# Optimization experiments

Hardware: AMD Instinct MI355X
Metric: run time of the kernel (lower is better)

Reference implementation:

```python
import jax, jax.numpy as jnp
import numpy as np
from functools import partial

# ---- constants from params ----
NODES = 64          # cfg_s[0]: nodes per graph
HEADS, BASES = 8, 4 # EGConv num_heads / num_bases (aggregators = ['symnorm'], A=1)
THRESH, LENS = 0.5, 0.5
ENC_THRESH, ENC_LENS = 0.5, 0.5
DECAY = 0.2
LSTM_ALPHA = 2.0

# ---- surrogate spike functions ----
@partial(jax.custom_vjp, nondiff_argnums=(1, 2))
def atan_spike(x, thresh, alpha):
    return (x > thresh).astype(x.dtype)

def _atan_fwd(x, thresh, alpha):
    return atan_spike(x, thresh, alpha), x

def _atan_bwd(thresh, alpha, x, g):
    grad = (alpha / 2.0) / (1.0 + (jnp.pi / 2.0 * alpha * (x - thresh)) ** 2)
    return (g * grad,)

atan_spike.defvjp(_atan_fwd, _atan_bwd)

@partial(jax.custom_vjp, nondiff_argnums=(1,))
def erf_spike(x, alpha):
    return (x > 0).astype(x.dtype)

def _erf_fwd(x, alpha):
    return erf_spike(x, alpha), x

def _erf_bwd(alpha, x, g):
    grad = alpha / (2.0 * jnp.sqrt(jnp.pi)) * jnp.exp(-(alpha * x / 2.0) ** 2)
    return (g * grad,)

erf_spike.defvjp(_erf_fwd, _erf_bwd)


def setup_inputs() -> dict:
    key = jax.random.key(0)
    N, Cin, T = 16384, 8, 32
    Cenc, Cgnn = 128, 128
    Fh = Cgnn // HEADS
    HID, FC1, NC = 512, 256, 4
    E = 262144
    ks = jax.random.split(key, 12)

    def w(k, shape, fan_in):
        return jax.random.normal(k, shape, jnp.float32) / np.float32(np.sqrt(fan_in))

    return {
        "x": jax.random.normal(ks[0], (N, Cin, T), jnp.float32),
        "edge_index": jax.random.randint(ks[1], (2, E), 0, N, dtype=jnp.int32),
        "enc_W": w(ks[2], (Cin, Cenc), Cin),
        "enc_b": jnp.zeros((Cenc,), jnp.float32),
        "bases_W": w(ks[3], (Cenc, BASES * Fh), Cenc),
        "bases_b": jnp.zeros((BASES * Fh,), jnp.float32),
        "comb_W": w(ks[4], (Cenc, HEADS * BASES), Cenc),
        "comb_b": jnp.zeros((HEADS * BASES,), jnp.float32),
        "conv_bias": jnp.zeros((Cgnn,), jnp.float32),
        "W_ih": w(ks[5], (NODES * Cgnn, 4 * HID), NODES * Cgnn),
        "W_hh": w(ks[6], (HID, 4 * HID), HID),
        "b_ih": jnp.zeros((4 * HID,), jnp.float32),
        "b_hh": jnp.zeros((4 * HID,), jnp.float32),
        "fc1_W": w(ks[7], (HID, FC1), HID),
        "fc1_b": jnp.zeros((FC1,), jnp.float32),
        "fc2_W": w(ks[8], (FC1, NC), FC1),
        "fc2_b": jnp.zeros((NC,), jnp.float32),
    }


def reference(x, edge_index, enc_W, enc_b, bases_W, bases_b, comb_W, comb_b,
              conv_bias, W_ih, W_hh, b_ih, b_hh, fc1_W, fc1_b, fc2_W, fc2_b):
    N, Cin, T = x.shape
    S = N // NODES
    Cgnn = conv_bias.shape[0]
    Fh = Cgnn // HEADS
    HID = W_hh.shape[0]
    FC1 = fc1_b.shape[0]
    NC = fc2_b.shape[0]

    # EGConv symnorm graph structure with self-loops (fixed across time)
    loop = jnp.arange(N, dtype=edge_index.dtype)
    s_all = jnp.concatenate([edge_index[0], loop])
    d_all = jnp.concatenate([edge_index[1], loop])
    deg = jax.ops.segment_sum(jnp.ones(s_all.shape[0], x.dtype), d_all, num_segments=N)
    dinv = jnp.where(deg > 0, jax.lax.rsqrt(jnp.maximum(deg, 1e-12)), 0.0)
    ew = dinv[s_all] * dinv[d_all]  # [E+N]

    xs = jnp.moveaxis(x, -1, 0)  # [T, N, Cin]

    def step(carry, xt):
        (enc_mem, enc_spike, c1_mem, c1_spike, lh, lc,
         h1_mem, h1_spike, h2_mem, h2_spike, h2_sum) = carry
        # encoding LIF
        enc_mem = enc_mem * DECAY * (1.0 - enc_spike) + xt @ enc_W + enc_b
        enc_spike = atan_spike(enc_mem, ENC_THRESH, ENC_LENS)
        # EGConv (symnorm aggregator, A=1)
        bases = enc_spike @ bases_W + bases_b                       # [N, B*Fh]
        agg = jax.ops.segment_sum(ew[:, None] * bases[s_all], d_all, num_segments=N)
        comb = (enc_spike @ comb_W + comb_b).reshape(N, HEADS, BASES)
        conv = jnp.einsum('nhb,nbf->nhf', comb, agg.reshape(N, BASES, Fh))
        conv = conv.reshape(S, NODES, Cgnn) + conv_bias
        # conv LIF
        c1_mem = c1_mem * DECAY * (1.0 - c1_spike) + conv
        c1_spike = atan_spike(c1_mem, THRESH, LENS)
        # spiking LSTM cell (erf surrogates on all gates)
        xl = c1_spike.reshape(S, NODES * Cgnn)
        gates = xl @ W_ih + b_ih + lh @ W_hh + b_hh
        i, f, g, o = jnp.split(gates, 4, axis=-1)
        i = erf_spike(i, LSTM_ALPHA)
        f = erf_spike(f, LSTM_ALPHA)
        g = erf_spike(g, LSTM_ALPHA)
        o = erf_spike(o, LSTM_ALPHA)
        lc = f * lc + i * g
        lh = lc * o
        # fc1 LIF
        h1_mem = h1_mem * DECAY * (1.0 - h1_spike) + lh @ fc1_W + fc1_b
        h1_spike = atan_spike(h1_mem, THRESH, LENS)
        # fc2 LIF
        h2_mem = h2_mem * DECAY * (1.0 - h2_spike) + h1_spike @ fc2_W + fc2_b
        h2_spike = atan_spike(h2_mem, THRESH, LENS)
        return (enc_mem, enc_spike, c1_mem, c1_spike, lh, lc,
                h1_mem, h1_spike, h2_mem, h2_spike, h2_sum + h2_spike), None

    Cenc = enc_b.shape[0]
    z = lambda shape: jnp.zeros(shape, x.dtype)
    carry0 = (z((N, Cenc)), z((N, Cenc)), z((S, NODES, Cgnn)), z((S, NODES, Cgnn)),
              z((S, HID)), z((S, HID)), z((S, FC1)), z((S, FC1)),
              z((S, NC)), z((S, NC)), z((S, NC)))
    carry, _ = jax.lax.scan(step, carry0, xs)
    h2_sum = carry[-1]
    return h2_sum / jnp.asarray(T, x.dtype)
```

## Files before the change

### kernel.cpp

```cpp
#include <hip/hip_runtime.h>

#define NN      16384
#define TSTEPS  32
#define SG      256
#define NE      262144
#define NPANEL  24
#define GSTRIDE 524288u

#define OFF_ENC_MEM   0u
#define OFF_ENC_SPK   2097152u
#define OFF_C1_MEM    4194304u
#define OFF_C1_SPK    6291456u
#define OFF_LH        8388608u
#define OFF_LC        8519680u
#define OFF_H1_MEM    8650752u
#define OFF_H1_SPK    8716288u
#define OFF_H2_MEM    8781824u
#define OFF_H2_SPK    8782848u
#define OFF_H2_SUM    8783872u
#define ZERO_FLOATS   8784896u
#define OFF_BASES     8784896u
#define OFF_COMB      9833472u
#define OFF_GATES     10357760u
#define OFF_PART      10882048u
#define OFF_DINV      23464960u
#define OFF_COLW      23481344u
#define FLOAT_END     23743488u
#define IOFF_DEG      0
#define IOFF_FILL     16384
#define IOFF_ROWPTR   32768
#define IOFF_EID      49153
#define IOFF_COL      311297
#define INT_COUNT     573441

__global__ void k_deg(const int* __restrict__ ei, int* __restrict__ deg) {
  int e = blockIdx.x * 256 + threadIdx.x;
  if (e < NE) atomicAdd(&deg[ei[NE + e]], 1);
}

__global__ void k_dinv(const int* __restrict__ deg, float* __restrict__ dinv) {
  int n = blockIdx.x * 256 + threadIdx.x;
  if (n < NN) dinv[n] = __fdiv_rn(1.0f, __fsqrt_rn((float)(deg[n] + 1)));
}

__global__ void k_scan(const int* __restrict__ deg, int* __restrict__ rowp) {
  __shared__ int sdata[1024];
  int tid = threadIdx.x;
  int base = tid * 16;
  int loc[16];
  int sum = 0;
  #pragma unroll
  for (int i = 0; i < 16; ++i) { loc[i] = sum; sum += deg[base + i]; }
  sdata[tid] = sum;
  __syncthreads();
  for (int off = 1; off < 1024; off <<= 1) {
    int v = 0;
    if (tid >= off) v = sdata[tid - off];
    __syncthreads();
    sdata[tid] += v;
    __syncthreads();
  }
  int excl = (tid == 0) ? 0 : sdata[tid - 1];
  #pragma unroll
  for (int i = 0; i < 16; ++i) rowp[base + i] = excl + loc[i];
  if (tid == 1023) rowp[NN] = sdata[1023];
}

__global__ void k_scatter(const int* __restrict__ ei, const int* __restrict__ rowp,
                          int* __restrict__ fill, int* __restrict__ eid) {
  int e = blockIdx.x * 256 + threadIdx.x;
  if (e >= NE) return;
  int d = ei[NE + e];
  int pos = rowp[d] + atomicAdd(&fill[d], 1);
  eid[pos] = e;
}

__global__ void k_sortadj(const int* __restrict__ rowp, int* __restrict__ eid,
                          const int* __restrict__ ei, const float* __restrict__ dinv,
                          int* __restrict__ col, float* __restrict__ colw) {
  int d = blockIdx.x * 256 + threadIdx.x;
  if (d >= NN) return;
  int r0 = rowp[d], r1 = rowp[d + 1];
  for (int i = r0 + 1; i < r1; ++i) {
    int key = eid[i];
    int j = i - 1;
    while (j >= r0 && eid[j] > key) { eid[j + 1] = eid[j]; --j; }
    eid[j + 1] = key;
  }
  for (int i = r0; i < r1; ++i) {
    int s = ei[eid[i]];
    col[i] = s;
    colw[i] = dinv[s];
  }
}

__global__ __launch_bounds__(512) void k_bases_comb(
    const float* __restrict__ x, const float* __restrict__ encW, const float* __restrict__ encB,
    float* __restrict__ enc_mem, float* __restrict__ enc_spk,
    const float* __restrict__ basesW, const float* __restrict__ basesB,
    const float* __restrict__ combW, const float* __restrict__ combB,
    float* __restrict__ bases, float* __restrict__ comb, int t) {
  __shared__ float xs[64][8];
  __shared__ float sp[64 * 129];
  __shared__ float ob[64 * 65];
  __shared__ float oc[64 * 33];
  const int tid = threadIdx.x;
  const int nb = blockIdx.x * 64;
  {
    int n = tid >> 3, c = tid & 7;
    xs[n][c] = x[(size_t)(nb + n) * 256 + (size_t)c * 32 + t];
  }
  __syncthreads();
  #pragma unroll 4
  for (int k = 0; k < 16; ++k) {
    int idx = k * 512 + tid;
    int n = idx >> 7, j = idx & 127;
    int gidx = nb * 128 + idx;
    float dot = 0.f;
    #pragma unroll
    for (int c = 0; c < 8; ++c) dot = __fmaf_rn(xs[n][c], encW[c * 128 + j], dot);
    float m = enc_mem[gidx], s = enc_spk[gidx];
    float nm = __fadd_rn(__fadd_rn(__fmul_rn(__fmul_rn(m, 0.2f), __fsub_rn(1.f, s)), dot), encB[j]);
    enc_mem[gidx] = nm;
    float spk = nm > 0.5f ? 1.f : 0.f;
    enc_spk[gidx] = spk;
    sp[n * 129 + j] = spk;
  }
  __syncthreads();
  const int lane = tid & 63;
  const int w = tid >> 6;
  const float* spn = sp + lane * 129;
  if (w < 4) {
    const int ch0 = w * 16;
    const float* Wp = basesW + ch0;
    float acc[16];
    #pragma unroll
    for (int c = 0; c < 16; ++c) acc[c] = 0.f;
    for (int j = 0; j < 128; ++j) {
      const float s = spn[j];
      const float* wr = Wp + j * 64;
      #pragma unroll
      for (int c = 0; c < 16; ++c) acc[c] = __fmaf_rn(s, wr[c], acc[c]);
    }
    #pragma unroll
    for (int c = 0; c < 16; ++c) ob[lane * 65 + ch0 + c] = acc[c];
  } else {
    const int ch0 = (w - 4) * 8;
    const float* Wp = combW + ch0;
    float acc[8];
    #pragma unroll
    for (int c = 0; c < 8; ++c) acc[c] = 0.f;
    for (int j = 0; j < 128; ++j) {
      const float s = spn[j];
      const float* wr = Wp + j * 32;
      #pragma unroll
      for (int c = 0; c < 8; ++c) acc[c] = __fmaf_rn(s, wr[c], acc[c]);
    }
    #pragma unroll
    for (int c = 0; c < 8; ++c) oc[lane * 33 + ch0 + c] = acc[c];
  }
  __syncthreads();
  #pragma unroll
  for (int r = 0; r < 8; ++r) {
    int idx = r * 512 + tid;
    int n = idx >> 6, ch = idx & 63;
    bases[(size_t)(nb + n) * 64 + ch] = __fadd_rn(ob[n * 65 + ch], basesB[ch]);
  }
  #pragma unroll
  for (int r = 0; r < 4; ++r) {
    int idx = r * 512 + tid;
    int n = idx >> 5, ch = idx & 31;
    comb[(size_t)(nb + n) * 32 + ch] = __fadd_rn(oc[n * 33 + ch], combB[ch]);
  }
}

__global__ __launch_bounds__(256) void k_aggconv(
    const float* __restrict__ bases, const float* __restrict__ comb,
    const float* __restrict__ dinv, const int* __restrict__ rowp,
    const int* __restrict__ col, const float* __restrict__ colw,
    const float* __restrict__ convB,
    float* __restrict__ c1_mem, float* __restrict__ c1_spk) {
  __shared__ float aggl[4][64];
  __shared__ float combl[4][32];
  int w = threadIdx.x >> 6;
  int m = threadIdx.x & 63;
  int d = blockIdx.x * 4 + w;
  float dd = dinv[d];
  int r0 = rowp[d], r1 = rowp[d + 1];
  float acc = 0.f;
  int r = r0;
  for (; r + 4 <= r1; r += 4) {
    const int s0 = col[r], s1 = col[r + 1], s2 = col[r + 2], s3 = col[r + 3];
    const float w0 = colw[r], w1 = colw[r + 1], w2 = colw[r + 2], w3 = colw[r + 3];
    const float b0 = bases[(size_t)s0 * 64 + m];
    const float b1 = bases[(size_t)s1 * 64 + m];
    const float b2 = bases[(size_t)s2 * 64 + m];
    const float b3 = bases[(size_t)s3 * 64 + m];
    acc = __fadd_rn(acc, __fmul_rn(__fmul_rn(w0, dd), b0));
    acc = __fadd_rn(acc, __fmul_rn(__fmul_rn(w1, dd), b1));
    acc = __fadd_rn(acc, __fmul_rn(__fmul_rn(w2, dd), b2));
    acc = __fadd_rn(acc, __fmul_rn(__fmul_rn(w3, dd), b3));
  }
  for (; r < r1; ++r) {
    int s = col[r];
    float ew  = __fmul_rn(colw[r], dd);
    float upd = __fmul_rn(ew, bases[(size_t)s * 64 + m]);
    acc = __fadd_rn(acc, upd);
  }
  {
    float ew  = __fmul_rn(dd, dd);
    float upd = __fmul_rn(ew, bases[(size_t)d * 64 + m]);
    acc = __fadd_rn(acc, upd);
  }
  aggl[w][m] = acc;
  if (m < 32) combl[w][m] = comb[(size_t)d * 32 + m];
  __syncthreads();
  #pragma unroll
  for (int half = 0; half < 2; ++half) {
    int j = m + half * 64;
    int h = j >> 4, f = j & 15;
    float cv = 0.f;
    #pragma unroll
    for (int b = 0; b < 4; ++b)
      cv = __fadd_rn(cv, __fmul_rn(combl[w][h * 4 + b], aggl[w][b * 16 + f]));
    cv = __fadd_rn(cv, convB[j]);
    int idx = d * 128 + j;
    float cm = c1_mem[idx], cs = c1_spk[idx];
    float nm = __fadd_rn(__fmul_rn(__fmul_rn(cm, 0.2f), __fsub_rn(1.f, cs)), cv);
    c1_mem[idx] = nm;
    c1_spk[idx] = nm > 0.5f ? 1.f : 0.f;
  }
}

__global__ __launch_bounds__(512) void k_gpanel(
    const float* __restrict__ xl, const float* __restrict__ lh,
    const float* __restrict__ Wih, const float* __restrict__ Whh,
    float* __restrict__ part) {
  __shared__ __align__(16) float Ast[2][16][132];
  __shared__ __align__(16) float Bs[2][16][132];
  const int tid = threadIdx.x;
  const int tx = tid & 31;
  const int ty = tid >> 5;
  const int n0 = blockIdx.x * 128;
  const int m0 = blockIdx.y * 128;
  const int z  = blockIdx.z;

  const float* Asrc; const float* Bsrc; int lda, k0, klen;
  if (z < 22) { Asrc = xl; Bsrc = Wih; lda = 8192; k0 = z * 384; klen = (z == 21) ? 128 : 384; }
  else        { Asrc = lh; Bsrc = Whh; lda = 512;  k0 = (z == 22) ? 0 : 384; klen = (z == 22) ? 384 : 128; }

  float acc[8][4];
  #pragma unroll
  for (int i = 0; i < 8; ++i)
    #pragma unroll
    for (int j = 0; j < 4; ++j) acc[i][j] = 0.f;

  const int arow = tid >> 2;
  const int acol = (tid & 3) * 4;
  const int brow = tid >> 5;
  const int bcol = (tid & 31) * 4;

  const int nkt = klen >> 4;

  float4 va, vb;

  va = *(const float4*)(Asrc + (size_t)(m0 + arow) * lda + k0 + acol);
  vb = *(const float4*)(Bsrc + (size_t)(k0 + brow) * 2048 + n0 + bcol);
  Ast[0][acol + 0][arow] = va.x; Ast[0][acol + 1][arow] = va.y;
  Ast[0][acol + 2][arow] = va.z; Ast[0][acol + 3][arow] = va.w;
  *(float4*)&Bs[0][brow][bcol] = vb;
  __syncthreads();

  for (int kt = 0; kt < nkt; ++kt) {
    const int cur = kt & 1;
    const bool more = (kt + 1 < nkt);
    if (more) {
      const int kb = k0 + ((kt + 1) << 4);
      va = *(const float4*)(Asrc + (size_t)(m0 + arow) * lda + kb + acol);
      vb = *(const float4*)(Bsrc + (size_t)(kb + brow) * 2048 + n0 + bcol);
    }
    #pragma unroll
    for (int kk = 0; kk < 16; ++kk) {
      const float4 a0 = *(const float4*)&Ast[cur][kk][ty * 8];
      const float4 a1 = *(const float4*)&Ast[cur][kk][ty * 8 + 4];
      const float4 b0 = *(const float4*)&Bs[cur][kk][tx * 4];
      const float av[8] = {a0.x, a0.y, a0.z, a0.w, a1.x, a1.y, a1.z, a1.w};
      const float bv[4] = {b0.x, b0.y, b0.z, b0.w};
      #pragma unroll
      for (int i = 0; i < 8; ++i)
        #pragma unroll
        for (int j = 0; j < 4; ++j)
          acc[i][j] = __fmaf_rn(av[i], bv[j], acc[i][j]);
    }
    if (more) {
      const int nxt = cur ^ 1;
      Ast[nxt][acol + 0][arow] = va.x; Ast[nxt][acol + 1][arow] = va.y;
      Ast[nxt][acol + 2][arow] = va.z; Ast[nxt][acol + 3][arow] = va.w;
      *(float4*)&Bs[nxt][brow][bcol] = vb;
      __syncthreads();
    }
  }

  float* dstz = part + (size_t)z * GSTRIDE + (size_t)m0 * 2048 + n0;
  #pragma unroll
  for (int i = 0; i < 8; ++i) {
    const int mr = ty * 8 + i;
    *(float4*)(dstz + (size_t)mr * 2048 + tx * 4) =
        make_float4(acc[i][0], acc[i][1], acc[i][2], acc[i][3]);
  }
}

__global__ __launch_bounds__(256) void k_combine(
    const float* __restrict__ part, const float* __restrict__ bih,
    const float* __restrict__ bhh, float* __restrict__ gates) {
  const int idx = blockIdx.x * 256 + threadIdx.x;
  const float* p = part + idx;
  float tih = p[0];
  #pragma unroll
  for (int zz = 1; zz < 22; ++zz) tih = __fadd_rn(tih, p[(size_t)zz * GSTRIDE]);
  const float thh = __fadd_rn(p[22u * GSTRIDE], p[23u * GSTRIDE]);
  const int u = idx & 2047;
  gates[idx] = __fadd_rn(__fadd_rn(__fadd_rn(tih, bih[u]), thh), bhh[u]);
}

__global__ __launch_bounds__(512) void k_cell(
    const float* __restrict__ gates,
    float* __restrict__ lc, float* __restrict__ lh,
    const float* __restrict__ fc1W, const float* __restrict__ fc1b,
    const float* __restrict__ fc2W, const float* __restrict__ fc2b,
    float* __restrict__ h1_mem, float* __restrict__ h1_spk,
    float* __restrict__ h2_mem, float* __restrict__ h2_spk, float* __restrict__ h2_sum) {
  __shared__ float lhl[512];
  __shared__ float a1buf[256];
  __shared__ float sp1l[256];
  const int s = blockIdx.x;
  const int tid = threadIdx.x;
  {
    const int h = tid;
    const float giv = gates[(size_t)s * 2048 + h];
    const float gfv = gates[(size_t)s * 2048 + 512 + h];
    const float ggv = gates[(size_t)s * 2048 + 1024 + h];
    const float gov = gates[(size_t)s * 2048 + 1536 + h];
    const float iv = giv > 0.f ? 1.f : 0.f;
    const float fv = gfv > 0.f ? 1.f : 0.f;
    const float gv = ggv > 0.f ? 1.f : 0.f;
    const float ov = gov > 0.f ? 1.f : 0.f;
    const int li = s * 512 + h;
    const float lcv = __fadd_rn(__fmul_rn(fv, lc[li]), __fmul_rn(iv, gv));
    lc[li] = lcv;
    const float lhv = __fmul_rn(lcv, ov);
    lh[li] = lhv;
    lhl[h] = lhv;
  }
  __syncthreads();
  float a0 = 0.f;
  if (tid < 256) {
    const int p = tid;
    #pragma unroll 8
    for (int q = 0; q < 384; ++q) a0 = __fmaf_rn(lhl[q], fc1W[q * 256 + p], a0);
  } else {
    const int p = tid - 256;
    float a1 = 0.f;
    #pragma unroll 8
    for (int q = 384; q < 512; ++q) a1 = __fmaf_rn(lhl[q], fc1W[q * 256 + p], a1);
    a1buf[p] = a1;
  }
  __syncthreads();
  if (tid < 256) {
    const int p = tid;
    const float dot1 = __fadd_rn(a0, a1buf[p]);
    const int i1 = s * 256 + p;
    const float m1 = h1_mem[i1], s1o = h1_spk[i1];
    const float nm1 = __fadd_rn(__fadd_rn(__fmul_rn(__fmul_rn(m1, 0.2f), __fsub_rn(1.f, s1o)), dot1), fc1b[p]);
    h1_mem[i1] = nm1;
    const float sp1 = nm1 > 0.5f ? 1.f : 0.f;
    h1_spk[i1] = sp1;
    sp1l[p] = sp1;
  }
  __syncthreads();
  if (tid < 4) {
    const int p = tid;
    float acc = 0.f;
    for (int q = 0; q < 256; ++q) acc = __fmaf_rn(sp1l[q], fc2W[q * 4 + p], acc);
    const int i2 = s * 4 + p;
    const float m2 = h2_mem[i2], s2o = h2_spk[i2];
    const float nm2 = __fadd_rn(__fadd_rn(__fmul_rn(__fmul_rn(m2, 0.2f), __fsub_rn(1.f, s2o)), acc), fc2b[p]);
    h2_mem[i2] = nm2;
    const float sp2 = nm2 > 0.5f ? 1.f : 0.f;
    h2_spk[i2] = sp2;
    h2_sum[i2] = __fadd_rn(h2_sum[i2], sp2);
  }
}

__global__ void k_out(const float* __restrict__ h2_sum, float* __restrict__ out) {
  int i = blockIdx.x * 256 + threadIdx.x;
  if (i < SG * 4) out[i] = __fmul_rn(h2_sum[i], 0.03125f);
}

extern "C" void kernel_launch(void* const* d_in, const int* in_sizes, int n_in,
                              void* d_out, int out_size, void* d_ws, size_t ws_size,
                              hipStream_t stream) {
  const float* x      = (const float*)d_in[0];
  const int*   ei     = (const int*)  d_in[1];
  const float* encW   = (const float*)d_in[2];
  const float* encB   = (const float*)d_in[3];
  const float* basesW = (const float*)d_in[4];
  const float* basesB = (const float*)d_in[5];
  const float* combW  = (const float*)d_in[6];
  const float* combB  = (const float*)d_in[7];
  const float* convB  = (const float*)d_in[8];
  const float* Wih    = (const float*)d_in[9];
  const float* Whh    = (const float*)d_in[10];
  const float* bih    = (const float*)d_in[11];
  const float* bhh    = (const float*)d_in[12];
  const float* fc1W   = (const float*)d_in[13];
  const float* fc1b   = (const float*)d_in[14];
  const float* fc2W   = (const float*)d_in[15];
  const float* fc2b   = (const float*)d_in[16];

  float* ws = (float*)d_ws;
  float* enc_mem = ws + OFF_ENC_MEM;
  float* enc_spk = ws + OFF_ENC_SPK;
  float* c1_mem  = ws + OFF_C1_MEM;
  float* c1_spk  = ws + OFF_C1_SPK;
  float* lhp     = ws + OFF_LH;
  float* lcp     = ws + OFF_LC;
  float* h1_mem  = ws + OFF_H1_MEM;
  float* h1_spk  = ws + OFF_H1_SPK;
  float* h2_mem  = ws + OFF_H2_MEM;
  float* h2_spk  = ws + OFF_H2_SPK;
  float* h2_sum  = ws + OFF_H2_SUM;
  float* bases   = ws + OFF_BASES;
  float* comb    = ws + OFF_COMB;
  float* gates   = ws + OFF_GATES;
  float* partp   = ws + OFF_PART;
  float* dinv    = ws + OFF_DINV;
  float* colw    = ws + OFF_COLW;
  int* ibase = (int*)((char*)d_ws + (size_t)FLOAT_END * 4);
  int* deg  = ibase + IOFF_DEG;
  int* fill = ibase + IOFF_FILL;
  int* rowp = ibase + IOFF_ROWPTR;
  int* eid  = ibase + IOFF_EID;
  int* col  = ibase + IOFF_COL;

  hipMemsetAsync(ws, 0, (size_t)ZERO_FLOATS * 4, stream);
  hipMemsetAsync(ibase, 0, 32768 * 4, stream);

  k_deg    <<<NE / 256, 256, 0, stream>>>(ei, deg);
  k_dinv   <<<NN / 256, 256, 0, stream>>>(deg, dinv);
  k_scan   <<<1, 1024, 0, stream>>>(deg, rowp);
  k_scatter<<<NE / 256, 256, 0, stream>>>(ei, rowp, fill, eid);
  k_sortadj<<<NN / 256, 256, 0, stream>>>(rowp, eid, ei, dinv, col, colw);

  for (int t = 0; t < TSTEPS; ++t) {
    k_bases_comb<<<NN / 64, 512, 0, stream>>>(x, encW, encB, enc_mem, enc_spk,
                                              basesW, basesB, combW, combB, bases, comb, t);
    k_aggconv   <<<NN / 4, 256, 0, stream>>>(bases, comb, dinv, rowp, col, colw, convB, c1_mem, c1_spk);
    k_gpanel    <<<dim3(16, 2, NPANEL), 512, 0, stream>>>(c1_spk, lhp, Wih, Whh, partp);
    k_combine   <<<2048, 256, 0, stream>>>(partp, bih, bhh, gates);
    k_cell      <<<SG, 512, 0, stream>>>(gates, lcp, lhp, fc1W, fc1b, fc2W, fc2b,
                                         h1_mem, h1_spk, h2_mem, h2_spk, h2_sum);
  }
  k_out<<<4, 256, 0, stream>>>(h2_sum, (float*)d_out);
}
```

Before: 6.122 ms.

## Use 8x8 register tiles and direct global-to-LDS loads in LSTM gate GEMM

Halves the gate-panel GEMM block to 256 threads, with each thread now computing an 8x8 output micro-tile (split into two 4-wide halves) instead of 8x4. This raises arithmetic intensity per LDS read. The B tile is now loaded with the global_load_lds builtin straight into shared memory, bypassing registers. This adds register pressure, and the async LDS loads rely on the existing barrier for ordering, which may be fragile.

```diff
diff --git a/kernel.cpp b/kernel.cpp
--- a/kernel.cpp
+++ b/kernel.cpp
@@ -232,15 +232,14 @@
   }
 }
 
-__global__ __launch_bounds__(512) void k_gpanel(
+__global__ __launch_bounds__(256) void k_gpanel(
     const float* __restrict__ xl, const float* __restrict__ lh,
     const float* __restrict__ Wih, const float* __restrict__ Whh,
     float* __restrict__ part) {
   __shared__ __align__(16) float Ast[2][16][132];
-  __shared__ __align__(16) float Bs[2][16][132];
+  __shared__ __align__(16) float Bs[2][16][128];
   const int tid = threadIdx.x;
-  const int tx = tid & 31;
-  const int ty = tid >> 5;
+  const int tx = tid & 15, ty = tid >> 4;
   const int n0 = blockIdx.x * 128;
   const int m0 = blockIdx.y * 128;
   const int z  = blockIdx.z;
@@ -249,26 +248,39 @@
   if (z < 22) { Asrc = xl; Bsrc = Wih; lda = 8192; k0 = z * 384; klen = (z == 21) ? 128 : 384; }
   else        { Asrc = lh; Bsrc = Whh; lda = 512;  k0 = (z == 22) ? 0 : 384; klen = (z == 22) ? 384 : 128; }
 
-  float acc[8][4];
+  float acc[8][8];
   #pragma unroll
   for (int i = 0; i < 8; ++i)
     #pragma unroll
-    for (int j = 0; j < 4; ++j) acc[i][j] = 0.f;
-
-  const int arow = tid >> 2;
-  const int acol = (tid & 3) * 4;
-  const int brow = tid >> 5;
-  const int bcol = (tid & 31) * 4;
+    for (int j = 0; j < 8; ++j) acc[i][j] = 0.f;
+
+  const int arow = tid >> 1;
+  const int acol = (tid & 1) * 8;
+  const int wid  = tid >> 6;
+  const int lane = tid & 63;
+  const int brow0 = wid * 4;
+  const int blr  = lane >> 5;
+  const int blc  = (lane & 31) * 4;
 
   const int nkt = klen >> 4;
-
-  float4 va, vb;
-
-  va = *(const float4*)(Asrc + (size_t)(m0 + arow) * lda + k0 + acol);
-  vb = *(const float4*)(Bsrc + (size_t)(k0 + brow) * 2048 + n0 + bcol);
-  Ast[0][acol + 0][arow] = va.x; Ast[0][acol + 1][arow] = va.y;
-  Ast[0][acol + 2][arow] = va.z; Ast[0][acol + 3][arow] = va.w;
-  *(float4*)&Bs[0][brow][bcol] = vb;
+  float4 va0, va1;
+
+  {
+    const float* srcA = Asrc + (size_t)(m0 + arow) * lda + k0 + acol;
+    va0 = ((const float4*)srcA)[0];
+    va1 = ((const float4*)srcA)[1];
+    const float* g0 = Bsrc + (size_t)(k0 + brow0 + blr) * 2048 + n0 + blc;
+    __builtin_amdgcn_global_load_lds(
+        (const __attribute__((address_space(1))) void*)g0,
+        (__attribute__((address_space(3))) void*)&Bs[0][brow0][0], 16, 0, 0);
+    __builtin_amdgcn_global_load_lds(
+        (const __attribute__((address_space(1))) void*)(g0 + 2 * 2048),
+        (__attribute__((address_space(3))) void*)&Bs[0][brow0 + 2][0], 16, 0, 0);
+    Ast[0][acol + 0][arow] = va0.x; Ast[0][acol + 1][arow] = va0.y;
+    Ast[0][acol + 2][arow] = va0.z; Ast[0][acol + 3][arow] = va0.w;
+    Ast[0][acol + 4][arow] = va1.x; Ast[0][acol + 5][arow] = va1.y;
+    Ast[0][acol + 6][arow] = va1.z; Ast[0][acol + 7][arow] = va1.w;
+  }
   __syncthreads();
 
   for (int kt = 0; kt < nkt; ++kt) {
@@ -276,27 +288,38 @@
     const bool more = (kt + 1 < nkt);
     if (more) {
       const int kb = k0 + ((kt + 1) << 4);
-      va = *(const float4*)(Asrc + (size_t)(m0 + arow) * lda + kb + acol);
-      vb = *(const float4*)(Bsrc + (size_t)(kb + brow) * 2048 + n0 + bcol);
+      const int nxt = cur ^ 1;
+      const float* g0 = Bsrc + (size_t)(kb + brow0 + blr) * 2048 + n0 + blc;
+      __builtin_amdgcn_global_load_lds(
+          (const __attribute__((address_space(1))) void*)g0,
+          (__attribute__((address_space(3))) void*)&Bs[nxt][brow0][0], 16, 0, 0);
+      __builtin_amdgcn_global_load_lds(
+          (const __attribute__((address_space(1))) void*)(g0 + 2 * 2048),
+          (__attribute__((address_space(3))) void*)&Bs[nxt][brow0 + 2][0], 16, 0, 0);
+      const float* srcA = Asrc + (size_t)(m0 + arow) * lda + kb + acol;
+      va0 = ((const float4*)srcA)[0];
+      va1 = ((const float4*)srcA)[1];
     }
     #pragma unroll
     for (int kk = 0; kk < 16; ++kk) {
-      const float4 a0 = *(const float4*)&Ast[cur][kk][ty * 8];
-      const float4 a1 = *(const float4*)&Ast[cur][kk][ty * 8 + 4];
+      const float4 a0 = *(const float4*)&Ast[cur][kk][ty * 4];
+      const float4 a1 = *(const float4*)&Ast[cur][kk][64 + ty * 4];
       const float4 b0 = *(const float4*)&Bs[cur][kk][tx * 4];
+      const float4 b1 = *(const float4*)&Bs[cur][kk][64 + tx * 4];
       const float av[8] = {a0.x, a0.y, a0.z, a0.w, a1.x, a1.y, a1.z, a1.w};
-      const float bv[4] = {b0.x, b0.y, b0.z, b0.w};
+      const float bv[8] = {b0.x, b0.y, b0.z, b0.w, b1.x, b1.y, b1.z, b1.w};
       #pragma unroll
       for (int i = 0; i < 8; ++i)
         #pragma unroll
-        for (int j = 0; j < 4; ++j)
+        for (int j = 0; j < 8; ++j)
           acc[i][j] = __fmaf_rn(av[i], bv[j], acc[i][j]);
     }
     if (more) {
       const int nxt = cur ^ 1;
-      Ast[nxt][acol + 0][arow] = va.x; Ast[nxt][acol + 1][arow] = va.y;
-      Ast[nxt][acol + 2][arow] = va.z; Ast[nxt][acol + 3][arow] = va.w;
-      *(float4*)&Bs[nxt][brow][bcol] = vb;
+      Ast[nxt][acol + 0][arow] = va0.x; Ast[nxt][acol + 1][arow] = va0.y;
+      Ast[nxt][acol + 2][arow] = va0.z; Ast[nxt][acol + 3][arow] = va0.w;
+      Ast[nxt][acol + 4][arow] = va1.x; Ast[nxt][acol + 5][arow] = va1.y;
+      Ast[nxt][acol + 6][arow] = va1.z; Ast[nxt][acol + 7][arow] = va1.w;
       __syncthreads();
     }
   }
@@ -304,9 +327,10 @@
   float* dstz = part + (size_t)z * GSTRIDE + (size_t)m0 * 2048 + n0;
   #pragma unroll
   for (int i = 0; i < 8; ++i) {
-    const int mr = ty * 8 + i;
-    *(float4*)(dstz + (size_t)mr * 2048 + tx * 4) =
-        make_float4(acc[i][0], acc[i][1], acc[i][2], acc[i][3]);
+    const int mr = ((i >> 2) << 6) + ty * 4 + (i & 3);
+    float* row = dstz + (size_t)mr * 2048;
+    *(float4*)(row + tx * 4)      = make_float4(acc[i][0], acc[i][1], acc[i][2], acc[i][3]);
+    *(float4*)(row + 64 + tx * 4) = make_float4(acc[i][4], acc[i][5], acc[i][6], acc[i][7]);
   }
 }
 
@@ -456,7 +480,7 @@
     k_bases_comb<<<NN / 64, 512, 0, stream>>>(x, encW, encB, enc_mem, enc_spk,
                                               basesW, basesB, combW, combB, bases, comb, t);
     k_aggconv   <<<NN / 4, 256, 0, stream>>>(bases, comb, dinv, rowp, col, colw, convB, c1_mem, c1_spk);
-    k_gpanel    <<<dim3(16, 2, NPANEL), 512, 0, stream>>>(c1_spk, lhp, Wih, Whh, partp);
+    k_gpanel    <<<dim3(16, 2, NPANEL), 256, 0, stream>>>(c1_spk, lhp, Wih, Whh, partp);
     k_combine   <<<2048, 256, 0, stream>>>(partp, bih, bhh, gates);
     k_cell      <<<SG, 512, 0, stream>>>(gates, lcp, lhp, fc1W, fc1b, fc2W, fc2b,
                                          h1_mem, h1_spk, h2_mem, h2_spk, h2_sum);
```

Result: slower. 7.909 ms (+29.2%).

## Replace dense split-K LSTM input GEMM with sparse spike-gather accumulation

Applied to the files above, without the earlier changes.

Each LSTM input row is a binary spike vector, so the new kernel compacts its nonzero indices into shared memory and sums only the matching W_ih rows, with no multiplies. The rounding order of the old 22 split-K panels is kept through the FOLD logic. The W_hh product and bias add move into the same kernel, which removes the partial buffer and the separate combine launch. The catch is that each of the 256 blocks streams scattered W_ih rows on its own, with no tile reuse across samples, so the cost now scales with spike density and depends on L2 reuse.

```diff
diff --git a/kernel.cpp b/kernel.cpp
--- a/kernel.cpp
+++ b/kernel.cpp
@@ -4,8 +4,6 @@
 #define TSTEPS  32
 #define SG      256
 #define NE      262144
-#define NPANEL  24
-#define GSTRIDE 524288u
 
 #define OFF_ENC_MEM   0u
 #define OFF_ENC_SPK   2097152u
@@ -22,7 +20,6 @@
 #define OFF_BASES     8784896u
 #define OFF_COMB      9833472u
 #define OFF_GATES     10357760u
-#define OFF_PART      10882048u
 #define OFF_DINV      23464960u
 #define OFF_COLW      23481344u
 #define FLOAT_END     23743488u
@@ -232,95 +229,125 @@
   }
 }
 
-__global__ __launch_bounds__(512) void k_gpanel(
+__global__ __launch_bounds__(512) void k_gates(
     const float* __restrict__ xl, const float* __restrict__ lh,
     const float* __restrict__ Wih, const float* __restrict__ Whh,
-    float* __restrict__ part) {
-  __shared__ __align__(16) float Ast[2][16][132];
-  __shared__ __align__(16) float Bs[2][16][132];
+    const float* __restrict__ bih, const float* __restrict__ bhh,
+    float* __restrict__ gates) {
+  __shared__ unsigned short nzk[8192];
+  __shared__ float lhs[512];
+  __shared__ int wsum[9];
   const int tid = threadIdx.x;
-  const int tx = tid & 31;
-  const int ty = tid >> 5;
-  const int n0 = blockIdx.x * 128;
-  const int m0 = blockIdx.y * 128;
-  const int z  = blockIdx.z;
-
-  const float* Asrc; const float* Bsrc; int lda, k0, klen;
-  if (z < 22) { Asrc = xl; Bsrc = Wih; lda = 8192; k0 = z * 384; klen = (z == 21) ? 128 : 384; }
-  else        { Asrc = lh; Bsrc = Whh; lda = 512;  k0 = (z == 22) ? 0 : 384; klen = (z == 22) ? 384 : 128; }
-
-  float acc[8][4];
-  #pragma unroll
-  for (int i = 0; i < 8; ++i)
-    #pragma unroll
-    for (int j = 0; j < 4; ++j) acc[i][j] = 0.f;
-
-  const int arow = tid >> 2;
-  const int acol = (tid & 3) * 4;
-  const int brow = tid >> 5;
-  const int bcol = (tid & 31) * 4;
-
-  const int nkt = klen >> 4;
-
-  float4 va, vb;
-
-  va = *(const float4*)(Asrc + (size_t)(m0 + arow) * lda + k0 + acol);
-  vb = *(const float4*)(Bsrc + (size_t)(k0 + brow) * 2048 + n0 + bcol);
-  Ast[0][acol + 0][arow] = va.x; Ast[0][acol + 1][arow] = va.y;
-  Ast[0][acol + 2][arow] = va.z; Ast[0][acol + 3][arow] = va.w;
-  *(float4*)&Bs[0][brow][bcol] = vb;
-  __syncthreads();
-
-  for (int kt = 0; kt < nkt; ++kt) {
-    const int cur = kt & 1;
-    const bool more = (kt + 1 < nkt);
-    if (more) {
-      const int kb = k0 + ((kt + 1) << 4);
-      va = *(const float4*)(Asrc + (size_t)(m0 + arow) * lda + kb + acol);
-      vb = *(const float4*)(Bsrc + (size_t)(kb + brow) * 2048 + n0 + bcol);
+  const int s = blockIdx.x;
+  const int lane = tid & 63, wv = tid >> 6;
+  const float* __restrict__ srow = xl + (size_t)s * 8192;
+
+  const int kb = tid * 16;
+  int cnt = 0;
+  #pragma unroll
+  for (int i = 0; i < 16; ++i) cnt += (srow[kb + i] != 0.f) ? 1 : 0;
+  int pfx = cnt;
+  #pragma unroll
+  for (int off = 1; off < 64; off <<= 1) {
+    int tval = __shfl_up(pfx, off);
+    if (lane >= off) pfx += tval;
+  }
+  if (lane == 63) wsum[wv] = pfx;
+  __syncthreads();
+  if (tid == 0) {
+    int a = 0;
+    #pragma unroll
+    for (int w = 0; w < 8; ++w) { int tv = wsum[w]; wsum[w] = a; a += tv; }
+    wsum[8] = a;
+  }
+  __syncthreads();
+  const int off0 = wsum[wv] + (pfx - cnt);
+  {
+    int c2 = 0;
+    #pragma unroll
+    for (int i = 0; i < 16; ++i) {
+      if (srow[kb + i] != 0.f) { nzk[off0 + c2] = (unsigned short)(kb + i); ++c2; }
     }
-    #pragma unroll
-    for (int kk = 0; kk < 16; ++kk) {
-      const float4 a0 = *(const float4*)&Ast[cur][kk][ty * 8];
-      const float4 a1 = *(const float4*)&Ast[cur][kk][ty * 8 + 4];
-      const float4 b0 = *(const float4*)&Bs[cur][kk][tx * 4];
-      const float av[8] = {a0.x, a0.y, a0.z, a0.w, a1.x, a1.y, a1.z, a1.w};
-      const float bv[4] = {b0.x, b0.y, b0.z, b0.w};
-      #pragma unroll
-      for (int i = 0; i < 8; ++i)
-        #pragma unroll
-        for (int j = 0; j < 4; ++j)
-          acc[i][j] = __fmaf_rn(av[i], bv[j], acc[i][j]);
-    }
-    if (more) {
-      const int nxt = cur ^ 1;
-      Ast[nxt][acol + 0][arow] = va.x; Ast[nxt][acol + 1][arow] = va.y;
-      Ast[nxt][acol + 2][arow] = va.z; Ast[nxt][acol + 3][arow] = va.w;
-      *(float4*)&Bs[nxt][brow][bcol] = vb;
-      __syncthreads();
-    }
-  }
-
-  float* dstz = part + (size_t)z * GSTRIDE + (size_t)m0 * 2048 + n0;
-  #pragma unroll
-  for (int i = 0; i < 8; ++i) {
-    const int mr = ty * 8 + i;
-    *(float4*)(dstz + (size_t)mr * 2048 + tx * 4) =
-        make_float4(acc[i][0], acc[i][1], acc[i][2], acc[i][3]);
-  }
-}
-
-__global__ __launch_bounds__(256) void k_combine(
-    const float* __restrict__ part, const float* __restrict__ bih,
-    const float* __restrict__ bhh, float* __restrict__ gates) {
-  const int idx = blockIdx.x * 256 + threadIdx.x;
-  const float* p = part + idx;
-  float tih = p[0];
-  #pragma unroll
-  for (int zz = 1; zz < 22; ++zz) tih = __fadd_rn(tih, p[(size_t)zz * GSTRIDE]);
-  const float thh = __fadd_rn(p[22u * GSTRIDE], p[23u * GSTRIDE]);
-  const int u = idx & 2047;
-  gates[idx] = __fadd_rn(__fadd_rn(__fadd_rn(tih, bih[u]), thh), bhh[u]);
+  }
+  lhs[tid] = lh[s * 512 + tid];
+  __syncthreads();
+  const int nnz = wsum[8];
+
+  const int cl = tid * 4;
+  const float* __restrict__ Wc = Wih + cl;
+  float4 tih = make_float4(0.f, 0.f, 0.f, 0.f);
+  float4 pz  = make_float4(0.f, 0.f, 0.f, 0.f);
+  int zcur = 0, pend = 384;
+
+#define FOLD(KK)                                                              \
+  while ((KK) >= pend) {                                                      \
+    tih.x = __fadd_rn(tih.x, pz.x); tih.y = __fadd_rn(tih.y, pz.y);           \
+    tih.z = __fadd_rn(tih.z, pz.z); tih.w = __fadd_rn(tih.w, pz.w);           \
+    pz.x = 0.f; pz.y = 0.f; pz.z = 0.f; pz.w = 0.f;                           \
+    ++zcur; pend = (zcur < 21) ? (pend + 384) : 8192;                         \
+  }
+
+  int k0_=0,k1_=0,k2_=0,k3_=0,k4_=0,k5_=0,k6_=0,k7_=0;
+  float4 w0_,w1_,w2_,w3_,w4_,w5_,w6_,w7_;
+#define PRELOAD(J, KS, WS)                                                    \
+  if ((J) < nnz) { KS = nzk[(J)]; WS = *(const float4*)(Wc + (size_t)KS * 2048); }
+  PRELOAD(0, k0_, w0_) PRELOAD(1, k1_, w1_) PRELOAD(2, k2_, w2_) PRELOAD(3, k3_, w3_)
+  PRELOAD(4, k4_, w4_) PRELOAD(5, k5_, w5_) PRELOAD(6, k6_, w6_) PRELOAD(7, k7_, w7_)
+
+#define STEP(KS, WS, BI, SO) {                                                \
+    const int kcur = KS; const float4 wv4 = WS;                               \
+    const int nidx = (BI) + (SO) + 8;                                         \
+    if (nidx < nnz) { KS = nzk[nidx]; WS = *(const float4*)(Wc + (size_t)KS * 2048); } \
+    FOLD(kcur);                                                               \
+    pz.x = __fadd_rn(pz.x, wv4.x); pz.y = __fadd_rn(pz.y, wv4.y);             \
+    pz.z = __fadd_rn(pz.z, wv4.z); pz.w = __fadd_rn(pz.w, wv4.w);             \
+  }
+
+  const int nmain = nnz & ~7;
+  for (int i = 0; i < nmain; i += 8) {
+    STEP(k0_, w0_, i, 0) STEP(k1_, w1_, i, 1) STEP(k2_, w2_, i, 2) STEP(k3_, w3_, i, 3)
+    STEP(k4_, w4_, i, 4) STEP(k5_, w5_, i, 5) STEP(k6_, w6_, i, 6) STEP(k7_, w7_, i, 7)
+  }
+  for (int i = nmain; i < nnz; ++i) {
+    const int kcur = nzk[i];
+    const float4 wv4 = *(const float4*)(Wc + (size_t)kcur * 2048);
+    FOLD(kcur);
+    pz.x = __fadd_rn(pz.x, wv4.x); pz.y = __fadd_rn(pz.y, wv4.y);
+    pz.z = __fadd_rn(pz.z, wv4.z); pz.w = __fadd_rn(pz.w, wv4.w);
+  }
+  for (; zcur < 22; ++zcur) {
+    tih.x = __fadd_rn(tih.x, pz.x); tih.y = __fadd_rn(tih.y, pz.y);
+    tih.z = __fadd_rn(tih.z, pz.z); tih.w = __fadd_rn(tih.w, pz.w);
+    pz.x = 0.f; pz.y = 0.f; pz.z = 0.f; pz.w = 0.f;
+  }
+#undef STEP
+#undef PRELOAD
+#undef FOLD
+
+  float4 p22 = make_float4(0.f, 0.f, 0.f, 0.f);
+  #pragma unroll 4
+  for (int k = 0; k < 384; ++k) {
+    const float sv = lhs[k];
+    const float4 wv4 = *(const float4*)(Whh + (size_t)k * 2048 + cl);
+    p22.x = __fmaf_rn(sv, wv4.x, p22.x); p22.y = __fmaf_rn(sv, wv4.y, p22.y);
+    p22.z = __fmaf_rn(sv, wv4.z, p22.z); p22.w = __fmaf_rn(sv, wv4.w, p22.w);
+  }
+  float4 p23 = make_float4(0.f, 0.f, 0.f, 0.f);
+  #pragma unroll 4
+  for (int k = 384; k < 512; ++k) {
+    const float sv = lhs[k];
+    const float4 wv4 = *(const float4*)(Whh + (size_t)k * 2048 + cl);
+    p23.x = __fmaf_rn(sv, wv4.x, p23.x); p23.y = __fmaf_rn(sv, wv4.y, p23.y);
+    p23.z = __fmaf_rn(sv, wv4.z, p23.z); p23.w = __fmaf_rn(sv, wv4.w, p23.w);
+  }
+  const float4 bi = *(const float4*)(bih + cl);
+  const float4 bh = *(const float4*)(bhh + cl);
+  float4 g;
+  g.x = __fadd_rn(__fadd_rn(__fadd_rn(tih.x, bi.x), __fadd_rn(p22.x, p23.x)), bh.x);
+  g.y = __fadd_rn(__fadd_rn(__fadd_rn(tih.y, bi.y), __fadd_rn(p22.y, p23.y)), bh.y);
+  g.z = __fadd_rn(__fadd_rn(__fadd_rn(tih.z, bi.z), __fadd_rn(p22.z, p23.z)), bh.z);
+  g.w = __fadd_rn(__fadd_rn(__fadd_rn(tih.w, bi.w), __fadd_rn(p22.w, p23.w)), bh.w);
+  *(float4*)(gates + (size_t)s * 2048 + cl) = g;
 }
 
 __global__ __launch_bounds__(512) void k_cell(
@@ -433,7 +460,6 @@
   float* bases   = ws + OFF_BASES;
   float* comb    = ws + OFF_COMB;
   float* gates   = ws + OFF_GATES;
-  float* partp   = ws + OFF_PART;
   float* dinv    = ws + OFF_DINV;
   float* colw    = ws + OFF_COLW;
   int* ibase = (int*)((char*)d_ws + (size_t)FLOAT_END * 4);
@@ -456,8 +482,7 @@
     k_bases_comb<<<NN / 64, 512, 0, stream>>>(x, encW, encB, enc_mem, enc_spk,
                                               basesW, basesB, combW, combB, bases, comb, t);
     k_aggconv   <<<NN / 4, 256, 0, stream>>>(bases, comb, dinv, rowp, col, colw, convB, c1_mem, c1_spk);
-    k_gpanel    <<<dim3(16, 2, NPANEL), 512, 0, stream>>>(c1_spk, lhp, Wih, Whh, partp);
-    k_combine   <<<2048, 256, 0, stream>>>(partp, bih, bhh, gates);
+    k_gates     <<<SG, 512, 0, stream>>>(c1_spk, lhp, Wih, Whh, bih, bhh, gates);
     k_cell      <<<SG, 512, 0, stream>>>(gates, lcp, lhp, fc1W, fc1b, fc2W, fc2b,
                                          h1_mem, h1_spk, h2_mem, h2_spk, h2_sum);
   }
```

Result: no change. 6.091 ms (-0.5%).

## Replace dense spike-by-W_ih GEMM with bitmask-driven sparse accumulation

Applied to the files above, without the earlier changes.

The input-to-hidden LSTM product multiplies binary spike activations by W_ih. The aggregation kernel now records which graphs spiked at each input feature in a per-feature bitmask using atomicOr. A new kernel reads each W_ih row once and adds it into LDS accumulators only for the graphs whose bit is set, which avoids the dense FMA work on zeros. The recurrent W_hh product stays a dense tiled GEMM in a separate kernel. In exchange the change adds global atomics and a mask clear each step, and the loop over set bits diverges within each wavefront.

```diff
diff --git a/kernel.cpp b/kernel.cpp
--- a/kernel.cpp
+++ b/kernel.cpp
@@ -4,7 +4,6 @@
 #define TSTEPS  32
 #define SG      256
 #define NE      262144
-#define NPANEL  24
 #define GSTRIDE 524288u
 
 #define OFF_ENC_MEM   0u
@@ -99,13 +98,15 @@
     float* __restrict__ enc_mem, float* __restrict__ enc_spk,
     const float* __restrict__ basesW, const float* __restrict__ basesB,
     const float* __restrict__ combW, const float* __restrict__ combB,
-    float* __restrict__ bases, float* __restrict__ comb, int t) {
+    float* __restrict__ bases, float* __restrict__ comb,
+    unsigned int* __restrict__ msk, int t) {
   __shared__ float xs[64][8];
   __shared__ float sp[64 * 129];
   __shared__ float ob[64 * 65];
   __shared__ float oc[64 * 33];
   const int tid = threadIdx.x;
   const int nb = blockIdx.x * 64;
+  if (tid < 256) msk[blockIdx.x * 256 + tid] = 0u;
   {
     int n = tid >> 3, c = tid & 7;
     xs[n][c] = x[(size_t)(nb + n) * 256 + (size_t)c * 32 + t];
@@ -179,7 +180,8 @@
     const float* __restrict__ dinv, const int* __restrict__ rowp,
     const int* __restrict__ col, const float* __restrict__ colw,
     const float* __restrict__ convB,
-    float* __restrict__ c1_mem, float* __restrict__ c1_spk) {
+    float* __restrict__ c1_mem, float* __restrict__ c1_spk,
+    unsigned int* __restrict__ msk) {
   __shared__ float aggl[4][64];
   __shared__ float combl[4][32];
   int w = threadIdx.x >> 6;
@@ -215,6 +217,8 @@
   aggl[w][m] = acc;
   if (m < 32) combl[w][m] = comb[(size_t)d * 32 + m];
   __syncthreads();
+  const int sg8 = d >> 6;
+  const int kbase = (d & 63) * 128;
   #pragma unroll
   for (int half = 0; half < 2; ++half) {
     int j = m + half * 64;
@@ -228,13 +232,50 @@
     float cm = c1_mem[idx], cs = c1_spk[idx];
     float nm = __fadd_rn(__fmul_rn(__fmul_rn(cm, 0.2f), __fsub_rn(1.f, cs)), cv);
     c1_mem[idx] = nm;
-    c1_spk[idx] = nm > 0.5f ? 1.f : 0.f;
-  }
-}
-
-__global__ __launch_bounds__(512) void k_gpanel(
-    const float* __restrict__ xl, const float* __restrict__ lh,
-    const float* __restrict__ Wih, const float* __restrict__ Whh,
+    float spk = nm > 0.5f ? 1.f : 0.f;
+    c1_spk[idx] = spk;
+    if (spk != 0.f)
+      atomicOr(&msk[(size_t)(kbase + j) * 8 + (sg8 >> 5)], 1u << (sg8 & 31));
+  }
+}
+
+__global__ __launch_bounds__(512) void k_gpart(
+    const float* __restrict__ Wih, const unsigned int* __restrict__ msk,
+    float* __restrict__ part) {
+  __shared__ float accl[256 * 32];
+  __shared__ unsigned int wm[8][384];
+  const int tid = threadIdx.x;
+  const int lane = tid & 63, wv = tid >> 6;
+  const int colc = lane & 31, half = lane >> 5;
+  const int cl = blockIdx.x * 32;
+  const int z = blockIdx.y;
+  const int k0 = z * 384;
+  const int klen = (z == 21) ? 128 : 384;
+
+  for (int i = tid; i < 256 * 32; i += 512) accl[i] = 0.f;
+  for (int k = lane; k < klen; k += 64) wm[wv][k] = msk[(size_t)(k0 + k) * 8 + wv];
+  __syncthreads();
+
+  const float* __restrict__ Wb = Wih + cl + colc;
+  #pragma unroll 4
+  for (int k = 0; k < klen; ++k) {
+    const float wval = Wb[(size_t)(k0 + k) * 2048];
+    unsigned int mh = (wm[wv][k] >> (half * 16)) & 0xffffu;
+    while (mh) {
+      const int b = __ffs(mh) - 1; mh &= mh - 1;
+      const int s = wv * 32 + half * 16 + b;
+      accl[s * 32 + colc] = __fadd_rn(accl[s * 32 + colc], wval);
+    }
+  }
+  #pragma unroll
+  for (int i = 0; i < 16; ++i) {
+    const int s = wv * 32 + half * 16 + i;
+    part[(size_t)z * GSTRIDE + (size_t)s * 2048 + cl + colc] = accl[s * 32 + colc];
+  }
+}
+
+__global__ __launch_bounds__(512) void k_gpanel_hh(
+    const float* __restrict__ lh, const float* __restrict__ Whh,
     float* __restrict__ part) {
   __shared__ __align__(16) float Ast[2][16][132];
   __shared__ __align__(16) float Bs[2][16][132];
@@ -243,11 +284,10 @@
   const int ty = tid >> 5;
   const int n0 = blockIdx.x * 128;
   const int m0 = blockIdx.y * 128;
-  const int z  = blockIdx.z;
-
-  const float* Asrc; const float* Bsrc; int lda, k0, klen;
-  if (z < 22) { Asrc = xl; Bsrc = Wih; lda = 8192; k0 = z * 384; klen = (z == 21) ? 128 : 384; }
-  else        { Asrc = lh; Bsrc = Whh; lda = 512;  k0 = (z == 22) ? 0 : 384; klen = (z == 22) ? 384 : 128; }
+  const int z2 = blockIdx.z;
+  const int k0 = z2 ? 384 : 0;
+  const int klen = z2 ? 128 : 384;
+  const int lda = 512;
 
   float acc[8][4];
   #pragma unroll
@@ -259,13 +299,11 @@
   const int acol = (tid & 3) * 4;
   const int brow = tid >> 5;
   const int bcol = (tid & 31) * 4;
-
   const int nkt = klen >> 4;
-
   float4 va, vb;
 
-  va = *(const float4*)(Asrc + (size_t)(m0 + arow) * lda + k0 + acol);
-  vb = *(const float4*)(Bsrc + (size_t)(k0 + brow) * 2048 + n0 + bcol);
+  va = *(const float4*)(lh + (size_t)(m0 + arow) * lda + k0 + acol);
+  vb = *(const float4*)(Whh + (size_t)(k0 + brow) * 2048 + n0 + bcol);
   Ast[0][acol + 0][arow] = va.x; Ast[0][acol + 1][arow] = va.y;
   Ast[0][acol + 2][arow] = va.z; Ast[0][acol + 3][arow] = va.w;
   *(float4*)&Bs[0][brow][bcol] = vb;
@@ -276,8 +314,8 @@
     const bool more = (kt + 1 < nkt);
     if (more) {
       const int kb = k0 + ((kt + 1) << 4);
-      va = *(const float4*)(Asrc + (size_t)(m0 + arow) * lda + kb + acol);
-      vb = *(const float4*)(Bsrc + (size_t)(kb + brow) * 2048 + n0 + bcol);
+      va = *(const float4*)(lh + (size_t)(m0 + arow) * lda + kb + acol);
+      vb = *(const float4*)(Whh + (size_t)(kb + brow) * 2048 + n0 + bcol);
     }
     #pragma unroll
     for (int kk = 0; kk < 16; ++kk) {
@@ -301,7 +339,7 @@
     }
   }
 
-  float* dstz = part + (size_t)z * GSTRIDE + (size_t)m0 * 2048 + n0;
+  float* dstz = part + (size_t)(22 + z2) * GSTRIDE + (size_t)m0 * 2048 + n0;
   #pragma unroll
   for (int i = 0; i < 8; ++i) {
     const int mr = ty * 8 + i;
@@ -442,6 +480,7 @@
   int* rowp = ibase + IOFF_ROWPTR;
   int* eid  = ibase + IOFF_EID;
   int* col  = ibase + IOFF_COL;
+  unsigned int* msk = (unsigned int*)(ibase + IOFF_EID);
 
   hipMemsetAsync(ws, 0, (size_t)ZERO_FLOATS * 4, stream);
   hipMemsetAsync(ibase, 0, 32768 * 4, stream);
@@ -454,9 +493,11 @@
 
   for (int t = 0; t < TSTEPS; ++t) {
     k_bases_comb<<<NN / 64, 512, 0, stream>>>(x, encW, encB, enc_mem, enc_spk,
-                                              basesW, basesB, combW, combB, bases, comb, t);
-    k_aggconv   <<<NN / 4, 256, 0, stream>>>(bases, comb, dinv, rowp, col, colw, convB, c1_mem, c1_spk);
-    k_gpanel    <<<dim3(16, 2, NPANEL), 512, 0, stream>>>(c1_spk, lhp, Wih, Whh, partp);
+                                              basesW, basesB, combW, combB, bases, comb, msk, t);
+    k_aggconv   <<<NN / 4, 256, 0, stream>>>(bases, comb, dinv, rowp, col, colw, convB,
+                                             c1_mem, c1_spk, msk);
+    k_gpart     <<<dim3(64, 22), 512, 0, stream>>>(Wih, msk, partp);
+    k_gpanel_hh <<<dim3(16, 2, 2), 512, 0, stream>>>(lhp, Whh, partp);
     k_combine   <<<2048, 256, 0, stream>>>(partp, bih, bhh, gates);
     k_cell      <<<SG, 512, 0, stream>>>(gates, lcp, lhp, fc1W, fc1b, fc2W, fc2b,
                                          h1_mem, h1_spk, h2_mem, h2_spk, h2_sum);
```

After: 10.58 ms. 1.73x slower.
